# Optimization experiments

Measured on AMD Instinct MI355X. Metric: run time of the kernel, lower is better.

## Reference

```python
import jax, jax.numpy as jnp
import numpy as np

B, T, D = 2, 1024, 4096
N, K, H = 32, 8, 128  # query heads, kv heads, head_dim
SLOTS = 4096
ROPE_THETA = 500000.0


def apply_rope(x, positions, head_dim, theta):
    # x: [B, heads, T, H], positions: [B, T]
    half = head_dim // 2
    inv_freq = 1.0 / (theta ** (jnp.arange(0, half, dtype=jnp.float32) / half * 2.0 * 0.5 * 2))
    inv_freq = 1.0 / (theta ** (jnp.arange(0, head_dim, 2, dtype=jnp.float32) / head_dim))  # [half]
    ang = positions.astype(jnp.float32)[:, :, None] * inv_freq[None, None, :]  # [B, T, half]
    cos = jnp.cos(ang)[:, None, :, :]  # [B, 1, T, half]
    sin = jnp.sin(ang)[:, None, :, :]
    x1, x2 = x[..., :half], x[..., half:]
    return jnp.concatenate([x1 * cos - x2 * sin, x2 * cos + x1 * sin], axis=-1)


def update_cache(cache, write_indices, kv):
    # cache: [K, SLOTS, H]; kv: [B, K, T, H]; write_indices: [B*T] flat slot ids
    flat = kv.transpose(1, 0, 2, 3).reshape(kv.shape[1], -1, kv.shape[3])  # [K, B*T, H]
    return cache.at[:, write_indices, :].set(flat)


def setup_inputs() -> dict:
    key = jax.random.key(0)
    ks = jax.random.split(key, 6)
    scale = 0.02
    x = jax.random.normal(ks[0], (B, T, D), jnp.float32)
    wq = jax.random.normal(ks[1], (N, D, H), jnp.float32) * scale
    wk = jax.random.normal(ks[2], (K, D, H), jnp.float32) * scale
    wv = jax.random.normal(ks[3], (K, D, H), jnp.float32) * scale
    wo = jax.random.normal(ks[4], (N, H, D), jnp.float32) * scale
    positions = jnp.tile(jnp.arange(T, dtype=jnp.int32)[None, :], (B, 1))
    k_cache = jnp.zeros((K, SLOTS, H), jnp.float32)
    v_cache = jnp.zeros((K, SLOTS, H), jnp.float32)
    write_indices = jnp.arange(B * T, dtype=jnp.int32)
    return {"x": x, "positions": positions, "wq": wq, "wk": wk, "wv": wv,
            "wo": wo, "k_cache": k_cache, "v_cache": v_cache,
            "write_indices": write_indices}


def reference(x, positions, wq, wk, wv, wo, k_cache, v_cache, write_indices):
    # QKV projections
    q = jnp.einsum('btd,ndh->bnth', x, wq)          # [B, N, T, H]
    k = jnp.einsum('btd,kdh->bkth', x, wk)          # [B, K, T, H]
    v = jnp.einsum('btd,kdh->bkth', x, wv)
    # RoPE, then scale q (matches module: rope before scaling)
    q = apply_rope(q, positions, H, ROPE_THETA) * (H ** -0.5)
    k = apply_rope(k, positions, H, ROPE_THETA)
    # KV-cache scatter update (prefill path)
    k_cache_new = update_cache(k_cache, write_indices, k)
    v_cache_new = update_cache(v_cache, write_indices, v)
    # GQA repeat + causal flash attention
    rep = N // K
    kr = jnp.repeat(k, rep, axis=1)                 # [B, N, T, H]
    vr = jnp.repeat(v, rep, axis=1)
    scores = jnp.einsum('bnth,bnsh->bnts', q, kr)   # [B, N, T, T]
    causal = jnp.tril(jnp.ones((T, T), bool))
    scores = jnp.where(causal[None, None], scores, jnp.finfo(scores.dtype).min)
    probs = jax.nn.softmax(scores, axis=-1)
    attn = jnp.einsum('bnts,bnsh->bnth', probs, vr) # [B, N, T, H]
    o = jnp.einsum('bnth,nhd->btd', attn, wo)       # [B, T, D]
    return (k_cache_new, v_cache_new, o)
```

## Files before the change

kernel.cpp:

```cpp
#include <hip/hip_runtime.h>

typedef unsigned short u16;
typedef float fx4 __attribute__((ext_vector_type(4)));
typedef __bf16 bfx8 __attribute__((ext_vector_type(8)));

#define TSEQ 1024
#define DMODEL 4096
#define NHEADS 32
#define KHEADS 8
#define HDIM 128
#define NSLOTS 4096
#define NEG_INF (-1e30f)

__device__ __forceinline__ u16 f2bf(float f) {
    union { float f; unsigned u; } v; v.f = f;
    unsigned u = v.u;
    unsigned r = (u + 0x7FFFu + ((u >> 16) & 1u)) >> 16;
    return (u16)r;
}
__device__ __forceinline__ float bf2f(u16 h) {
    union { unsigned u; float f; } v; v.u = ((unsigned)h) << 16; return v.f;
}
__device__ __forceinline__ void gll16(const void* g, void* l) {
    __builtin_amdgcn_global_load_lds((__attribute__((address_space(1))) void*)(g),
                                     (__attribute__((address_space(3))) void*)(l),
                                     16, 0, 0);
}

__global__ __launch_bounds__(256) void cvt_bf16(const float* __restrict__ in,
                                                u16* __restrict__ out, int n) {
    int i = (blockIdx.x * 256 + threadIdx.x) * 8;
    if (i >= n) return;
    float4 a = *(const float4*)(in + i);
    float4 b = *(const float4*)(in + i + 4);
    u16 tmp[8] = {f2bf(a.x), f2bf(a.y), f2bf(a.z), f2bf(a.w),
                  f2bf(b.x), f2bf(b.y), f2bf(b.z), f2bf(b.w)};
    *(uint4*)(out + i) = *(uint4*)tmp;
}

__global__ __launch_bounds__(256) void transpose_w(const float* __restrict__ in,
                                                   u16* __restrict__ out,
                                                   int R, int C) {
    __shared__ __align__(16) u16 t[64][72];
    const float* ih = in + (size_t)blockIdx.z * R * C;
    u16* oh = out + (size_t)blockIdx.z * R * C;
    int r0 = blockIdx.y * 64, c0 = blockIdx.x * 64;
    int tid = threadIdx.x;
    int rr = tid >> 4, c4 = tid & 15;
#pragma unroll
    for (int i = 0; i < 4; ++i) {
        int r = rr + i * 16;
        float4 v = *(const float4*)(ih + (size_t)(r0 + r) * C + c0 + c4 * 4);
        t[c4 * 4 + 0][r] = f2bf(v.x);
        t[c4 * 4 + 1][r] = f2bf(v.y);
        t[c4 * 4 + 2][r] = f2bf(v.z);
        t[c4 * 4 + 3][r] = f2bf(v.w);
    }
    __syncthreads();
    int rr2 = tid >> 3, c8 = tid & 7;
#pragma unroll
    for (int i = 0; i < 2; ++i) {
        int r = rr2 + i * 32;
        *(uint4*)(oh + (size_t)(c0 + r) * R + r0 + c8 * 8) = *(uint4*)&t[r][c8 * 8];
    }
}

template <int OUTF32>
__global__ __launch_bounds__(256) void gemm_bt(const u16* __restrict__ A,
                                               const u16* __restrict__ Bt,
                                               void* __restrict__ Cv,
                                               int M, int N, int Kd) {
    __shared__ __align__(16) u16 As[128 * 64];
    __shared__ __align__(16) u16 Bs[128 * 64];
    const int tid = threadIdx.x;
    const int lane = tid & 63;
    const int wave = tid >> 6;
    const int wm = (wave >> 1) * 64;
    const int wn = (wave & 1) * 64;
    const int m0 = blockIdx.y * 128;
    const int n0 = blockIdx.x * 128;
    const int quad = lane >> 4;
    const int l15 = lane & 15;
    const int srow = lane >> 3;
    const int sc8 = (lane & 7) ^ srow;

    fx4 zero = {0.f, 0.f, 0.f, 0.f};
    fx4 acc[4][4];
#pragma unroll
    for (int i = 0; i < 4; ++i)
#pragma unroll
        for (int j = 0; j < 4; ++j) acc[i][j] = zero;

    for (int k0 = 0; k0 < Kd; k0 += 64) {
        __syncthreads();
#pragma unroll
        for (int i = 0; i < 4; ++i) {
            int c = wave * 4 + i;
            gll16(A + (size_t)(m0 + c * 8 + srow) * Kd + (k0 + sc8 * 8), &As[c * 512]);
            gll16(Bt + (size_t)(n0 + c * 8 + srow) * Kd + (k0 + sc8 * 8), &Bs[c * 512]);
        }
        __syncthreads();
#pragma unroll
        for (int ks = 0; ks < 2; ++ks) {
            bfx8 af[4], bf[4];
#pragma unroll
            for (int t = 0; t < 4; ++t) {
                int row = wm + t * 16 + l15;
                int r7 = row & 7;
                int k8 = (ks * 4 + quad) ^ r7;
                af[t] = *(const bfx8*)&As[(row >> 3) * 512 + r7 * 64 + k8 * 8];
                int rowb = wn + t * 16 + l15;
                int r7b = rowb & 7;
                int k8b = (ks * 4 + quad) ^ r7b;
                bf[t] = *(const bfx8*)&Bs[(rowb >> 3) * 512 + r7b * 64 + k8b * 8];
            }
#pragma unroll
            for (int tm = 0; tm < 4; ++tm)
#pragma unroll
                for (int tn = 0; tn < 4; ++tn)
                    acc[tm][tn] = __builtin_amdgcn_mfma_f32_16x16x32_bf16(
                        af[tm], bf[tn], acc[tm][tn], 0, 0, 0);
        }
    }
#pragma unroll
    for (int tm = 0; tm < 4; ++tm)
#pragma unroll
        for (int tn = 0; tn < 4; ++tn) {
            int col = n0 + wn + tn * 16 + l15;
#pragma unroll
            for (int r = 0; r < 4; ++r) {
                int row = m0 + wm + tm * 16 + quad * 4 + r;
                if (OUTF32)
                    ((float*)Cv)[(size_t)row * N + col] = acc[tm][tn][r];
                else
                    ((u16*)Cv)[(size_t)row * N + col] = f2bf(acc[tm][tn][r]);
            }
        }
}

__global__ __launch_bounds__(256) void rope_scatter(
    const u16* __restrict__ qkv, const int* __restrict__ positions,
    const int* __restrict__ wi, u16* __restrict__ qb, u16* __restrict__ kb,
    u16* __restrict__ vb, float* __restrict__ kcache, float* __restrict__ vcache) {
    int m = blockIdx.y;
    int j = blockIdx.x * 256 + threadIdx.x;
    int head = j >> 7, h = j & 127;
    int b = m >> 10, t = m & 1023;
    float self = bf2f(qkv[(size_t)m * 6144 + j]);
    if (head < 40) {
        int i = h & 63;
        float invf = __expf(-0.20503693f * (float)i);
        float ang = (float)positions[m] * invf;
        float c, s;
        __sincosf(ang, &s, &c);
        float other = bf2f(qkv[(size_t)m * 6144 + (j ^ 64)]);
        float out = (h < 64) ? (self * c - other * s) : (self * c + other * s);
        if (head < 32) {
            out *= 0.08838834764831845f;
            qb[((size_t)(b * 32 + head) * 1024 + t) * 128 + h] = f2bf(out);
        } else {
            int kh = head - 32;
            kb[((size_t)(b * 8 + kh) * 1024 + t) * 128 + h] = f2bf(out);
            kcache[((size_t)kh * NSLOTS + wi[m]) * 128 + h] = out;
        }
    } else {
        int kh = head - 40;
        vb[((size_t)(b * 8 + kh) * 1024 + t) * 128 + h] = f2bf(self);
        vcache[((size_t)kh * NSLOTS + wi[m]) * 128 + h] = self;
    }
}

__global__ __launch_bounds__(256) void transpose_v(const u16* __restrict__ vb,
                                                   u16* __restrict__ vt) {
    int gid = blockIdx.x * 256 + threadIdx.x;
    int t8 = gid & 127;
    int h = (gid >> 7) & 127;
    int bk = gid >> 14;
    const u16* src = vb + (size_t)bk * 131072;
    u16 tmp[8];
#pragma unroll
    for (int j = 0; j < 8; ++j) tmp[j] = src[(size_t)(t8 * 8 + j) * 128 + h];
    *(uint4*)(vt + (size_t)bk * 131072 + (size_t)h * 1024 + t8 * 8) = *(uint4*)tmp;
}

__global__ __launch_bounds__(256) void flash_attn(const u16* __restrict__ qb,
                                                  const u16* __restrict__ kb,
                                                  const u16* __restrict__ vt,
                                                  u16* __restrict__ attn) {
    const int qt = blockIdx.x;
    const int n = blockIdx.y;
    const int b = blockIdx.z;
    const int kh = n >> 2;
    const int tid = threadIdx.x;
    const int lane = tid & 63;
    const int wave = tid >> 6;
    const int quad = lane >> 4;
    const int l15 = lane & 15;

    __shared__ __align__(16) u16 Ks[64 * 136];
    __shared__ __align__(16) u16 Vs[128 * 72];
    __shared__ __align__(16) u16 Ps[4][16 * 72];

    const u16* qbase =
        qb + ((size_t)(b * 32 + n) * 1024 + qt * 64 + wave * 16 + l15) * 128;
    bfx8 qf[4];
#pragma unroll
    for (int ks = 0; ks < 4; ++ks)
        qf[ks] = *(const bfx8*)(qbase + ks * 32 + quad * 8);

    const u16* kbase = kb + (size_t)(b * 8 + kh) * 1024 * 128;
    const u16* vbase = vt + (size_t)(b * 8 + kh) * 128 * 1024;

    fx4 zero = {0.f, 0.f, 0.f, 0.f};
    fx4 o[8];
#pragma unroll
    for (int i = 0; i < 8; ++i) o[i] = zero;
    float mrow[4], lrow[4];
#pragma unroll
    for (int r = 0; r < 4; ++r) { mrow[r] = NEG_INF; lrow[r] = 0.f; }

    for (int kt = 0; kt <= qt; ++kt) {
        __syncthreads();
        {
            int rr = tid >> 4, c8 = tid & 15;
#pragma unroll
            for (int i = 0; i < 4; ++i) {
                int row = rr + i * 16;
                *(uint4*)&Ks[row * 136 + c8 * 8] =
                    *(const uint4*)(kbase + (size_t)(kt * 64 + row) * 128 + c8 * 8);
            }
        }
        {
            int rr = tid >> 3, c8 = tid & 7;
#pragma unroll
            for (int i = 0; i < 4; ++i) {
                int row = rr + i * 32;
                *(uint4*)&Vs[row * 72 + c8 * 8] =
                    *(const uint4*)(vbase + (size_t)row * 1024 + kt * 64 + c8 * 8);
            }
        }
        __syncthreads();
        fx4 sAcc[4];
#pragma unroll
        for (int t = 0; t < 4; ++t) sAcc[t] = zero;
#pragma unroll
        for (int ks = 0; ks < 4; ++ks)
#pragma unroll
            for (int tn = 0; tn < 4; ++tn) {
                bfx8 kf = *(const bfx8*)&Ks[(tn * 16 + l15) * 136 + ks * 32 + quad * 8];
                sAcc[tn] = __builtin_amdgcn_mfma_f32_16x16x32_bf16(qf[ks], kf,
                                                                   sAcc[tn], 0, 0, 0);
            }
        if (kt == qt) {
#pragma unroll
            for (int tn = 0; tn < 4; ++tn)
#pragma unroll
                for (int r = 0; r < 4; ++r) {
                    int qrow = wave * 16 + quad * 4 + r;
                    int krow = tn * 16 + l15;
                    if (krow > qrow) sAcc[tn][r] = NEG_INF;
                }
        }
        float alpha[4];
#pragma unroll
        for (int r = 0; r < 4; ++r) {
            float mx = fmaxf(fmaxf(sAcc[0][r], sAcc[1][r]),
                             fmaxf(sAcc[2][r], sAcc[3][r]));
#pragma unroll
            for (int d = 1; d < 16; d <<= 1) mx = fmaxf(mx, __shfl_xor(mx, d));
            float mnew = fmaxf(mrow[r], mx);
            alpha[r] = __expf(mrow[r] - mnew);
            mrow[r] = mnew;
            float rs = 0.f;
#pragma unroll
            for (int tn = 0; tn < 4; ++tn) {
                float p = __expf(sAcc[tn][r] - mnew);
                sAcc[tn][r] = p;
                rs += p;
            }
#pragma unroll
            for (int d = 1; d < 16; d <<= 1) rs += __shfl_xor(rs, d);
            lrow[r] = lrow[r] * alpha[r] + rs;
        }
#pragma unroll
        for (int tn = 0; tn < 4; ++tn)
#pragma unroll
            for (int r = 0; r < 4; ++r)
                Ps[wave][(quad * 4 + r) * 72 + tn * 16 + l15] = f2bf(sAcc[tn][r]);
#pragma unroll
        for (int ht = 0; ht < 8; ++ht)
#pragma unroll
            for (int r = 0; r < 4; ++r) o[ht][r] *= alpha[r];
        __syncthreads();
#pragma unroll
        for (int ks2 = 0; ks2 < 2; ++ks2) {
            bfx8 pf = *(const bfx8*)&Ps[wave][l15 * 72 + ks2 * 32 + quad * 8];
#pragma unroll
            for (int ht = 0; ht < 8; ++ht) {
                bfx8 vf = *(const bfx8*)&Vs[(ht * 16 + l15) * 72 + ks2 * 32 + quad * 8];
                o[ht] = __builtin_amdgcn_mfma_f32_16x16x32_bf16(pf, vf, o[ht], 0, 0, 0);
            }
        }
    }
    float inv_l[4];
#pragma unroll
    for (int r = 0; r < 4; ++r) inv_l[r] = 1.f / lrow[r];
#pragma unroll
    for (int ht = 0; ht < 8; ++ht)
#pragma unroll
        for (int r = 0; r < 4; ++r) {
            int t = qt * 64 + wave * 16 + quad * 4 + r;
            int col = n * 128 + ht * 16 + l15;
            attn[((size_t)(b * 1024 + t)) * 4096 + col] = f2bf(o[ht][r] * inv_l[r]);
        }
}

extern "C" void kernel_launch(void* const* d_in, const int* in_sizes, int n_in,
                              void* d_out, int out_size, void* d_ws, size_t ws_size,
                              hipStream_t stream) {
    const float* x = (const float*)d_in[0];
    const int* pos = (const int*)d_in[1];
    const float* wq = (const float*)d_in[2];
    const float* wk = (const float*)d_in[3];
    const float* wv = (const float*)d_in[4];
    const float* wo = (const float*)d_in[5];
    const float* kc = (const float*)d_in[6];
    const float* vc = (const float*)d_in[7];
    const int* wi = (const int*)d_in[8];

    float* kc_out = (float*)d_out;
    float* vc_out = kc_out + 4194304;
    float* o_out = vc_out + 4194304;

    u16* wsp = (u16*)d_ws;
    u16* x_bf  = wsp;
    u16* wqkvT = x_bf + 8388608;
    u16* woT   = wqkvT + 25165824;
    u16* qkv   = woT + 16777216;
    u16* qbuf  = qkv + 12582912;
    u16* kbuf  = qbuf + 8388608;
    u16* vbuf  = kbuf + 2097152;
    u16* vtb   = vbuf + 2097152;
    u16* attn  = vtb + 2097152;

    hipMemcpyAsync(kc_out, kc, (size_t)4194304 * 4, hipMemcpyDeviceToDevice, stream);
    hipMemcpyAsync(vc_out, vc, (size_t)4194304 * 4, hipMemcpyDeviceToDevice, stream);

    cvt_bf16<<<4096, 256, 0, stream>>>(x, x_bf, 8388608);
    transpose_w<<<dim3(2, 64, 32), 256, 0, stream>>>(wq, wqkvT, 4096, 128);
    transpose_w<<<dim3(2, 64, 8), 256, 0, stream>>>(wk, wqkvT + 16777216, 4096, 128);
    transpose_w<<<dim3(2, 64, 8), 256, 0, stream>>>(wv, wqkvT + 20971520, 4096, 128);
    transpose_w<<<dim3(64, 64, 1), 256, 0, stream>>>(wo, woT, 4096, 4096);

    gemm_bt<0><<<dim3(48, 16), 256, 0, stream>>>(x_bf, wqkvT, qkv, 2048, 6144, 4096);
    rope_scatter<<<dim3(24, 2048), 256, 0, stream>>>(qkv, pos, wi, qbuf, kbuf, vbuf,
                                                     kc_out, vc_out);
    transpose_v<<<1024, 256, 0, stream>>>(vbuf, vtb);
    flash_attn<<<dim3(16, 32, 2), 256, 0, stream>>>(qbuf, kbuf, vtb, attn);
    gemm_bt<1><<<dim3(32, 16), 256, 0, stream>>>(attn, woT, o_out, 2048, 4096, 4096);
}
```

Measured before the change: 572.8 us.

## Use direct-to-LDS swizzled loads in attention, fuse V transpose and QKV weight transposes

Flash attention now loads K and V tiles with global_load_lds into XOR-swizzled unpadded LDS, removes one barrier per tile, and uses exp2 with log2e folded into the q scale. Rope/scatter processes two elements per thread and no longer materialises a separate V buffer. A tiled LDS transpose builds V^T directly from the qkv buffer, and the three QKV weight transposes are merged into one launch. This aims to cut global memory traffic, launch overhead and LDS bank conflicts, at the risk of per-wave Ps hazards from the removed sync.

```diff
diff --git a/kernel.cpp b/kernel.cpp
--- a/kernel.cpp
+++ b/kernel.cpp
@@ -4,13 +4,9 @@
 typedef float fx4 __attribute__((ext_vector_type(4)));
 typedef __bf16 bfx8 __attribute__((ext_vector_type(8)));
 
-#define TSEQ 1024
-#define DMODEL 4096
-#define NHEADS 32
-#define KHEADS 8
-#define HDIM 128
 #define NSLOTS 4096
 #define NEG_INF (-1e30f)
+#define QSCALE 0.12751879523486166f
 
 __device__ __forceinline__ u16 f2bf(float f) {
     union { float f; unsigned u; } v; v.f = f;
@@ -38,13 +34,10 @@
     *(uint4*)(out + i) = *(uint4*)tmp;
 }
 
-__global__ __launch_bounds__(256) void transpose_w(const float* __restrict__ in,
-                                                   u16* __restrict__ out,
-                                                   int R, int C) {
+__device__ __forceinline__ void transpose_body(const float* __restrict__ ih,
+                                               u16* __restrict__ oh, int R, int C,
+                                               int r0, int c0) {
     __shared__ __align__(16) u16 t[64][72];
-    const float* ih = in + (size_t)blockIdx.z * R * C;
-    u16* oh = out + (size_t)blockIdx.z * R * C;
-    int r0 = blockIdx.y * 64, c0 = blockIdx.x * 64;
     int tid = threadIdx.x;
     int rr = tid >> 4, c4 = tid & 15;
 #pragma unroll
@@ -63,6 +56,25 @@
         int r = rr2 + i * 32;
         *(uint4*)(oh + (size_t)(c0 + r) * R + r0 + c8 * 8) = *(uint4*)&t[r][c8 * 8];
     }
+}
+
+__global__ __launch_bounds__(256) void transpose_w(const float* __restrict__ in,
+                                                   u16* __restrict__ out,
+                                                   int R, int C) {
+    transpose_body(in + (size_t)blockIdx.z * R * C, out + (size_t)blockIdx.z * R * C,
+                   R, C, blockIdx.y * 64, blockIdx.x * 64);
+}
+
+__global__ __launch_bounds__(256) void transpose_wqkv(const float* __restrict__ wq,
+                                                      const float* __restrict__ wk,
+                                                      const float* __restrict__ wv,
+                                                      u16* __restrict__ out) {
+    int z = blockIdx.z;
+    const float* in = (z < 32) ? wq + (size_t)z * 524288
+                               : (z < 40) ? wk + (size_t)(z - 32) * 524288
+                                          : wv + (size_t)(z - 40) * 524288;
+    transpose_body(in, out + (size_t)z * 524288, 4096, 128, blockIdx.y * 64,
+                   blockIdx.x * 64);
 }
 
 template <int OUTF32>
@@ -141,46 +153,80 @@
 __global__ __launch_bounds__(256) void rope_scatter(
     const u16* __restrict__ qkv, const int* __restrict__ positions,
     const int* __restrict__ wi, u16* __restrict__ qb, u16* __restrict__ kb,
-    u16* __restrict__ vb, float* __restrict__ kcache, float* __restrict__ vcache) {
+    float* __restrict__ kcache, float* __restrict__ vcache) {
     int m = blockIdx.y;
-    int j = blockIdx.x * 256 + threadIdx.x;
-    int head = j >> 7, h = j & 127;
+    int j2 = blockIdx.x * 256 + threadIdx.x;
+    int head = j2 >> 6;
+    int hp = (j2 & 63) * 2;
     int b = m >> 10, t = m & 1023;
-    float self = bf2f(qkv[(size_t)m * 6144 + j]);
+    const u16* row = qkv + (size_t)m * 6144 + head * 128;
+    unsigned sv = *(const unsigned*)(row + hp);
+    float v0 = bf2f((u16)sv), v1 = bf2f((u16)(sv >> 16));
     if (head < 40) {
-        int i = h & 63;
-        float invf = __expf(-0.20503693f * (float)i);
-        float ang = (float)positions[m] * invf;
-        float c, s;
-        __sincosf(ang, &s, &c);
-        float other = bf2f(qkv[(size_t)m * 6144 + (j ^ 64)]);
-        float out = (h < 64) ? (self * c - other * s) : (self * c + other * s);
+        int i = hp & 63;
+        float p = (float)positions[m];
+        float ang0 = p * __expf(-0.20503693f * (float)i);
+        float ang1 = ang0 * 0.81461709f;
+        float c0, s0, c1, s1;
+        __sincosf(ang0, &s0, &c0);
+        __sincosf(ang1, &s1, &c1);
+        unsigned ov = *(const unsigned*)(row + (hp ^ 64));
+        float w0 = bf2f((u16)ov), w1 = bf2f((u16)(ov >> 16));
+        float o0, o1;
+        if (hp < 64) { o0 = v0 * c0 - w0 * s0; o1 = v1 * c1 - w1 * s1; }
+        else         { o0 = v0 * c0 + w0 * s0; o1 = v1 * c1 + w1 * s1; }
         if (head < 32) {
-            out *= 0.08838834764831845f;
-            qb[((size_t)(b * 32 + head) * 1024 + t) * 128 + h] = f2bf(out);
+            o0 *= QSCALE; o1 *= QSCALE;
+            u16 t2[2] = {f2bf(o0), f2bf(o1)};
+            *(unsigned*)(qb + ((size_t)(b * 32 + head) * 1024 + t) * 128 + hp) =
+                *(unsigned*)t2;
         } else {
             int kh = head - 32;
-            kb[((size_t)(b * 8 + kh) * 1024 + t) * 128 + h] = f2bf(out);
-            kcache[((size_t)kh * NSLOTS + wi[m]) * 128 + h] = out;
+            u16 t2[2] = {f2bf(o0), f2bf(o1)};
+            *(unsigned*)(kb + ((size_t)(b * 8 + kh) * 1024 + t) * 128 + hp) =
+                *(unsigned*)t2;
+            float2 f2 = {o0, o1};
+            *(float2*)(kcache + ((size_t)kh * NSLOTS + wi[m]) * 128 + hp) = f2;
         }
     } else {
         int kh = head - 40;
-        vb[((size_t)(b * 8 + kh) * 1024 + t) * 128 + h] = f2bf(self);
-        vcache[((size_t)kh * NSLOTS + wi[m]) * 128 + h] = self;
-    }
-}
-
-__global__ __launch_bounds__(256) void transpose_v(const u16* __restrict__ vb,
-                                                   u16* __restrict__ vt) {
-    int gid = blockIdx.x * 256 + threadIdx.x;
-    int t8 = gid & 127;
-    int h = (gid >> 7) & 127;
-    int bk = gid >> 14;
-    const u16* src = vb + (size_t)bk * 131072;
-    u16 tmp[8];
-#pragma unroll
-    for (int j = 0; j < 8; ++j) tmp[j] = src[(size_t)(t8 * 8 + j) * 128 + h];
-    *(uint4*)(vt + (size_t)bk * 131072 + (size_t)h * 1024 + t8 * 8) = *(uint4*)tmp;
+        float2 f2 = {v0, v1};
+        *(float2*)(vcache + ((size_t)kh * NSLOTS + wi[m]) * 128 + hp) = f2;
+    }
+}
+
+__global__ __launch_bounds__(256) void transpose_v2(const u16* __restrict__ qkv,
+                                                    u16* __restrict__ vt) {
+    __shared__ __align__(16) u16 Ts[64 * 64];
+    int tt = blockIdx.x;
+    int hh = blockIdx.y;
+    int bkh = blockIdx.z;
+    int bq = bkh >> 3, kh = bkh & 7;
+    int tid = threadIdx.x;
+    const u16* src =
+        qkv + (size_t)(bq * 1024 + tt * 64) * 6144 + 5120 + kh * 128 + hh * 64;
+    {
+        int r = tid >> 3, c8 = tid & 7;
+#pragma unroll
+        for (int i = 0; i < 2; ++i) {
+            int rr = r + i * 32;
+            *(uint4*)&Ts[rr * 64 + ((c8 ^ (rr & 7)) * 8)] =
+                *(const uint4*)(src + (size_t)rr * 6144 + c8 * 8);
+        }
+    }
+    __syncthreads();
+    int h = tid & 63, t8 = tid >> 6;
+    int h8 = h >> 3, h7 = h & 7;
+    u16* dst = vt + (size_t)bkh * 131072 + (size_t)(hh * 64 + h) * 1024 + tt * 64;
+#pragma unroll
+    for (int i = 0; i < 2; ++i) {
+        int tb = t8 + i * 4;
+        u16 tmp[8];
+#pragma unroll
+        for (int j = 0; j < 8; ++j)
+            tmp[j] = Ts[(tb * 8 + j) * 64 + ((h8 ^ j) * 8 + h7)];
+        *(uint4*)(dst + tb * 8) = *(uint4*)tmp;
+    }
 }
 
 __global__ __launch_bounds__(256) void flash_attn(const u16* __restrict__ qb,
@@ -197,8 +243,8 @@
     const int quad = lane >> 4;
     const int l15 = lane & 15;
 
-    __shared__ __align__(16) u16 Ks[64 * 136];
-    __shared__ __align__(16) u16 Vs[128 * 72];
+    __shared__ __align__(16) u16 Ks[64 * 128];
+    __shared__ __align__(16) u16 Vs[128 * 64];
     __shared__ __align__(16) u16 Ps[4][16 * 72];
 
     const u16* qbase =
@@ -208,8 +254,13 @@
     for (int ks = 0; ks < 4; ++ks)
         qf[ks] = *(const bfx8*)(qbase + ks * 32 + quad * 8);
 
-    const u16* kbase = kb + (size_t)(b * 8 + kh) * 1024 * 128;
-    const u16* vbase = vt + (size_t)(b * 8 + kh) * 128 * 1024;
+    const u16* kbase = kb + (size_t)(b * 8 + kh) * 131072;
+    const u16* vbase = vt + (size_t)(b * 8 + kh) * 131072;
+
+    const int kl = wave * 4 + (lane >> 4);
+    const int kh8 = (lane & 15) ^ (kl & 7);
+    const int hl = wave * 8 + (lane >> 3);
+    const int vk8 = (lane & 7) ^ (hl & 7);
 
     fx4 zero = {0.f, 0.f, 0.f, 0.f};
     fx4 o[8];
@@ -221,25 +272,18 @@
 
     for (int kt = 0; kt <= qt; ++kt) {
         __syncthreads();
-        {
-            int rr = tid >> 4, c8 = tid & 15;
-#pragma unroll
-            for (int i = 0; i < 4; ++i) {
-                int row = rr + i * 16;
-                *(uint4*)&Ks[row * 136 + c8 * 8] =
-                    *(const uint4*)(kbase + (size_t)(kt * 64 + row) * 128 + c8 * 8);
-            }
-        }
-        {
-            int rr = tid >> 3, c8 = tid & 7;
-#pragma unroll
-            for (int i = 0; i < 4; ++i) {
-                int row = rr + i * 32;
-                *(uint4*)&Vs[row * 72 + c8 * 8] =
-                    *(const uint4*)(vbase + (size_t)row * 1024 + kt * 64 + c8 * 8);
-            }
-        }
+        const u16* ksrc = kbase + (size_t)kt * 64 * 128;
+        const u16* vsrc = vbase + kt * 64;
+#pragma unroll
+        for (int i = 0; i < 4; ++i)
+            gll16(ksrc + (size_t)(i * 16 + kl) * 128 + kh8 * 8,
+                  &Ks[(i * 16 + wave * 4) * 128]);
+#pragma unroll
+        for (int i = 0; i < 4; ++i)
+            gll16(vsrc + (size_t)(i * 32 + hl) * 1024 + vk8 * 8,
+                  &Vs[(i * 32 + wave * 8) * 64]);
         __syncthreads();
+
         fx4 sAcc[4];
 #pragma unroll
         for (int t = 0; t < 4; ++t) sAcc[t] = zero;
@@ -247,7 +291,9 @@
         for (int ks = 0; ks < 4; ++ks)
 #pragma unroll
             for (int tn = 0; tn < 4; ++tn) {
-                bfx8 kf = *(const bfx8*)&Ks[(tn * 16 + l15) * 136 + ks * 32 + quad * 8];
+                int key = tn * 16 + l15;
+                bfx8 kf =
+                    *(const bfx8*)&Ks[key * 128 + (((ks * 4 + quad) ^ (key & 7)) * 8)];
                 sAcc[tn] = __builtin_amdgcn_mfma_f32_16x16x32_bf16(qf[ks], kf,
                                                                    sAcc[tn], 0, 0, 0);
             }
@@ -269,12 +315,12 @@
 #pragma unroll
             for (int d = 1; d < 16; d <<= 1) mx = fmaxf(mx, __shfl_xor(mx, d));
             float mnew = fmaxf(mrow[r], mx);
-            alpha[r] = __expf(mrow[r] - mnew);
+            alpha[r] = exp2f(mrow[r] - mnew);
             mrow[r] = mnew;
             float rs = 0.f;
 #pragma unroll
             for (int tn = 0; tn < 4; ++tn) {
-                float p = __expf(sAcc[tn][r] - mnew);
+                float p = exp2f(sAcc[tn][r] - mnew);
                 sAcc[tn][r] = p;
                 rs += p;
             }
@@ -291,13 +337,14 @@
         for (int ht = 0; ht < 8; ++ht)
 #pragma unroll
             for (int r = 0; r < 4; ++r) o[ht][r] *= alpha[r];
-        __syncthreads();
 #pragma unroll
         for (int ks2 = 0; ks2 < 2; ++ks2) {
             bfx8 pf = *(const bfx8*)&Ps[wave][l15 * 72 + ks2 * 32 + quad * 8];
 #pragma unroll
             for (int ht = 0; ht < 8; ++ht) {
-                bfx8 vf = *(const bfx8*)&Vs[(ht * 16 + l15) * 72 + ks2 * 32 + quad * 8];
+                int h = ht * 16 + l15;
+                bfx8 vf =
+                    *(const bfx8*)&Vs[h * 64 + (((ks2 * 4 + quad) ^ (h & 7)) * 8)];
                 o[ht] = __builtin_amdgcn_mfma_f32_16x16x32_bf16(pf, vf, o[ht], 0, 0, 0);
             }
         }
@@ -339,23 +386,20 @@
     u16* qkv   = woT + 16777216;
     u16* qbuf  = qkv + 12582912;
     u16* kbuf  = qbuf + 8388608;
-    u16* vbuf  = kbuf + 2097152;
-    u16* vtb   = vbuf + 2097152;
+    u16* vtb   = kbuf + 2097152;
     u16* attn  = vtb + 2097152;
 
     hipMemcpyAsync(kc_out, kc, (size_t)4194304 * 4, hipMemcpyDeviceToDevice, stream);
     hipMemcpyAsync(vc_out, vc, (size_t)4194304 * 4, hipMemcpyDeviceToDevice, stream);
 
     cvt_bf16<<<4096, 256, 0, stream>>>(x, x_bf, 8388608);
-    transpose_w<<<dim3(2, 64, 32), 256, 0, stream>>>(wq, wqkvT, 4096, 128);
-    transpose_w<<<dim3(2, 64, 8), 256, 0, stream>>>(wk, wqkvT + 16777216, 4096, 128);
-    transpose_w<<<dim3(2, 64, 8), 256, 0, stream>>>(wv, wqkvT + 20971520, 4096, 128);
+    transpose_wqkv<<<dim3(2, 64, 48), 256, 0, stream>>>(wq, wk, wv, wqkvT);
     transpose_w<<<dim3(64, 64, 1), 256, 0, stream>>>(wo, woT, 4096, 4096);
 
     gemm_bt<0><<<dim3(48, 16), 256, 0, stream>>>(x_bf, wqkvT, qkv, 2048, 6144, 4096);
-    rope_scatter<<<dim3(24, 2048), 256, 0, stream>>>(qkv, pos, wi, qbuf, kbuf, vbuf,
+    rope_scatter<<<dim3(12, 2048), 256, 0, stream>>>(qkv, pos, wi, qbuf, kbuf,
                                                      kc_out, vc_out);
-    transpose_v<<<1024, 256, 0, stream>>>(vbuf, vtb);
+    transpose_v2<<<dim3(16, 2, 16), 256, 0, stream>>>(qkv, vtb);
     flash_attn<<<dim3(16, 32, 2), 256, 0, stream>>>(qbuf, kbuf, vtb, attn);
     gemm_bt<1><<<dim3(32, 16), 256, 0, stream>>>(attn, woT, o_out, 2048, 4096, 4096);
 }
```

Result: faster. 542.7 us (-5.3%).
